# Performance work log

Hardware: AMD Instinct MI355X
Metric: run time of the kernel (lower is better)

## Reference

```python
import jax, jax.numpy as jnp
import numpy as np


def setup_inputs() -> dict:
    key = jax.random.key(0)
    ks = jax.random.split(key, 8)
    B, S, H, I = 2, 1025, 3200, 12800
    T = B * S
    # int8 tensors represented as int32, symmetric range [-128, 126]
    hidden_states = jax.random.randint(ks[0], (B, S, H), 0, 255, dtype=jnp.int32) - 127
    scale_in = (jax.random.uniform(ks[1], (T,)) * 0.02 + 1e-4).astype(jnp.float16)
    w1 = jax.random.randint(ks[2], (I, H), 0, 255, dtype=jnp.int32) - 127
    w1_scale = (jax.random.uniform(ks[3], (I,)) * 0.01 + 1e-4).astype(jnp.float32)
    b1 = (jax.random.normal(ks[4], (I,)) * 0.02).astype(jnp.float16)
    w2 = jax.random.randint(ks[5], (H, I), 0, 255, dtype=jnp.int32) - 127
    w2_scale = (jax.random.uniform(ks[6], (H,)) * 0.01 + 1e-4).astype(jnp.float32)
    b2 = (jax.random.normal(ks[7], (H,)) * 0.02).astype(jnp.float16)
    return {"hidden_states": hidden_states, "scale_in": scale_in,
            "w1": w1, "w1_scale": w1_scale, "b1": b1,
            "w2": w2, "w2_scale": w2_scale, "b2": b2}


def _w8a8_linear(x_int, scale_x, w_int, w_scale, bias):
    # int8 GEMM with int32 accumulation, dequant with per-token * per-channel scales
    acc = jnp.matmul(x_int, w_int.T)  # [T, out] int32
    out = acc.astype(jnp.float32) * scale_x[:, None].astype(jnp.float32) * w_scale[None, :]
    return (out + bias.astype(jnp.float32)).astype(jnp.float16)


def _gelu_and_quant(x_f16):
    # fused GELU + per-token dynamic symmetric int8 quantization
    g = jax.nn.gelu(x_f16.astype(jnp.float32), approximate=False)  # [T, I]
    amax = jnp.max(jnp.abs(g), axis=-1)                              # [T]
    scale_act = (amax / 127.0).astype(jnp.float16)
    s = jnp.maximum(scale_act.astype(jnp.float32), 1e-8)
    q = jnp.clip(jnp.round(g / s[:, None]), -128, 127).astype(jnp.int32)
    return q, scale_act


def reference(hidden_states, scale_in, w1, w1_scale, b1, w2, w2_scale, b2):
    B, S, H = hidden_states.shape
    x = hidden_states.reshape(-1, H)               # [T, H] int
    fc1_out = _w8a8_linear(x, scale_in, w1, w1_scale, b1)      # [T, I] fp16
    act_out, scale_act = _gelu_and_quant(fc1_out)              # int8-as-int32, [T] fp16
    fc2_out = _w8a8_linear(act_out, scale_act, w2, w2_scale, b2)  # [T, H] fp16
    return fc2_out
```

## Files before the change

### kernel.cpp

```cpp
#include <hip/hip_runtime.h>
#include <hip/hip_fp16.h>

typedef int v4i __attribute__((ext_vector_type(4)));

#define AS1C(p) ((const __attribute__((address_space(1))) void*)(p))
#define AS3(p)  ((__attribute__((address_space(3))) void*)(p))

__global__ void pack1(const int* __restrict__ a, const int* __restrict__ b,
                      signed char* __restrict__ pa, signed char* __restrict__ pb,
                      unsigned int* __restrict__ amax,
                      long long na, long long nb, int T) {
  const long long gid = blockIdx.x * (long long)blockDim.x + threadIdx.x;
  if (gid < T) amax[gid] = 0u;
  const long long n4a = na >> 2, n4b = nb >> 2;
  const long long tot = n4a + n4b;
  const long long stride = (long long)gridDim.x * blockDim.x;
  for (long long u = gid; u < tot; u += stride) {
    const int* src; signed char* dst; long long loc;
    if (u < n4a) { src = a; dst = pa; loc = u; }
    else         { src = b; dst = pb; loc = u - n4a; }
    const int4 v = *(const int4*)(src + (loc << 2));
    const unsigned out = (unsigned)(v.x & 0xff) | ((unsigned)(v.y & 0xff) << 8) |
                         ((unsigned)(v.z & 0xff) << 16) | ((unsigned)(v.w & 0xff) << 24);
    *(unsigned*)(dst + (loc << 2)) = out;
  }
}

__launch_bounds__(1024, 4)
__global__ void fc1_fused(const signed char* __restrict__ A, const signed char* __restrict__ Bw,
                          int M, int N, int K,
                          const float* __restrict__ scale_tok, const float* __restrict__ wsc,
                          const float* __restrict__ bias,
                          __half* __restrict__ gout, unsigned int* __restrict__ amax,
                          const int* __restrict__ w2src, signed char* __restrict__ w2dst,
                          long long n4w2, int npack, int gy) {
  __shared__ __align__(16) char smem[2][32768];
  const int bid = blockIdx.x;

  if (bid < npack) {
    const long long stride = (long long)npack * 1024;
    for (long long u = (long long)bid * 1024 + threadIdx.x; u < n4w2; u += stride) {
      const int4 v = *(const int4*)(w2src + (u << 2));
      const unsigned out = (unsigned)(v.x & 0xff) | ((unsigned)(v.y & 0xff) << 8) |
                           ((unsigned)(v.z & 0xff) << 16) | ((unsigned)(v.w & 0xff) << 24);
      *(unsigned*)(w2dst + (u << 2)) = out;
    }
    return;
  }

  const int tid = threadIdx.x;
  const int lane = tid & 63, wave = tid >> 6;
  const int wavem = wave >> 2, waven = wave & 3;
  const int lh = lane & 15, sseg = lane >> 4;

  int lid;
  {
    const int o = bid - npack;
    const int nwg = gridDim.x - npack;
    const int q = nwg >> 3, r = nwg & 7;
    const int x = o & 7, p = o >> 3;
    lid = (x < r ? x * (q + 1) : r * (q + 1) + (x - r) * q) + p;
  }
  const long long t0 = (long long)(lid % gy) * 256;
  const long long n0 = (long long)(lid / gy) * 256;
  const int nk = K >> 6;
  const long long Mm1 = M - 1, Nm1 = N - 1;

  const int lr4 = lane >> 2, slot = lane & 3;
  const int rloc = wave * 16 + lr4;
  const int gslot = (slot ^ ((rloc >> 1) & 3)) << 4;
  const signed char* sp0;
  const signed char* sp1;
  {
    long long gr = t0 + rloc; if (gr > Mm1) gr = Mm1;
    sp0 = A + gr * (long long)K + gslot;
    long long gn = n0 + rloc; if (gn > Nm1) gn = Nm1;
    sp1 = Bw + gn * (long long)K + gslot;
  }
  const int d0 = wave * 1024, d1 = 16384 + wave * 1024;

#define STAGE(bi) do { \
    __builtin_amdgcn_global_load_lds(AS1C(sp0), AS3(&smem[bi][d0]), 16, 0, 0); sp0 += 64; \
    __builtin_amdgcn_global_load_lds(AS1C(sp1), AS3(&smem[bi][d1]), 16, 0, 0); sp1 += 64; \
  } while (0)

  const int xs = ((sseg ^ ((lh >> 1) & 3)) << 4);
  const int offA = wavem * 4096 + lh * 64 + xs;
  const int offB = 16384 + waven * 4096 + lh * 64 + xs;

  v4i acc[4][4] = {};

  STAGE(0);
  __syncthreads();

  int cur = 0;
  for (int kt = 0; kt < nk; ++kt) {
    if (kt + 1 < nk) STAGE(cur ^ 1);
    const char* base = smem[cur];
    v4i af[4], bf[2];
#pragma unroll
    for (int mi = 0; mi < 4; ++mi) af[mi] = *(const v4i*)(base + offA + mi * 1024);
    bf[0] = *(const v4i*)(base + offB);
    bf[1] = *(const v4i*)(base + offB + 1024);
#pragma unroll
    for (int mi = 0; mi < 4; ++mi) {
      acc[mi][0] = __builtin_amdgcn_mfma_i32_16x16x64_i8(af[mi], bf[0], acc[mi][0], 0, 0, 0);
      acc[mi][1] = __builtin_amdgcn_mfma_i32_16x16x64_i8(af[mi], bf[1], acc[mi][1], 0, 0, 0);
    }
    bf[0] = *(const v4i*)(base + offB + 2048);
    bf[1] = *(const v4i*)(base + offB + 3072);
#pragma unroll
    for (int mi = 0; mi < 4; ++mi) {
      acc[mi][2] = __builtin_amdgcn_mfma_i32_16x16x64_i8(af[mi], bf[0], acc[mi][2], 0, 0, 0);
      acc[mi][3] = __builtin_amdgcn_mfma_i32_16x16x64_i8(af[mi], bf[1], acc[mi][3], 0, 0, 0);
    }
    __syncthreads();
    cur ^= 1;
  }
#undef STAGE

  long long cidx[4]; float w4[4], bi4[4]; bool cok[4];
#pragma unroll
  for (int ni = 0; ni < 4; ++ni) {
    cidx[ni] = n0 + waven * 64 + ni * 16 + lh;
    cok[ni] = cidx[ni] < N;
    w4[ni] = cok[ni] ? wsc[cidx[ni]] : 0.f;
    bi4[ni] = cok[ni] ? bias[cidx[ni]] : 0.f;
  }
#pragma unroll
  for (int mi = 0; mi < 4; ++mi) {
#pragma unroll
    for (int j = 0; j < 4; ++j) {
      const long long t = t0 + wavem * 64 + mi * 16 + (lane >> 4) * 4 + j;
      const bool valid = t < M;
      const float st = valid ? scale_tok[t] : 0.f;
      float rowmax = 0.f;
#pragma unroll
      for (int ni = 0; ni < 4; ++ni) {
        float v = (float)acc[mi][ni][j] * st * w4[ni] + bi4[ni];
        v = __half2float(__float2half(v));
        const float gl = 0.5f * v * (1.f + erff(v * 0.70710678118654752f));
        rowmax = fmaxf(rowmax, fabsf(gl));
        if (valid && cok[ni]) gout[t * (long long)N + cidx[ni]] = __float2half(gl);
      }
#pragma unroll
      for (int m = 1; m < 16; m <<= 1) rowmax = fmaxf(rowmax, __shfl_xor(rowmax, m));
      if (valid && lh == 0) atomicMax(&amax[t], __float_as_uint(rowmax));
    }
  }
}

__launch_bounds__(256, 4)
__global__ void gemm_fc2s(const signed char* __restrict__ A, const signed char* __restrict__ Bw,
                          int M, int N, int K, int* __restrict__ pbuf) {
  __shared__ __align__(16) char lds[2][2][128 * 64];
  const int tid = threadIdx.x;
  const int lane = tid & 63, wave = tid >> 6;
  const int wrow = (wave >> 1) * 64, wcol = (wave & 1) * 64;

  const int z = blockIdx.x & 1;
  const int o = blockIdx.x >> 1;
  const int gy = (M + 127) >> 7;
  const int nwg = gridDim.x >> 1;
  int lid;
  {
    const int q = nwg >> 3, r = nwg & 7;
    const int x = o & 7, p = o >> 3;
    lid = (x < r ? x * (q + 1) : r * (q + 1) + (x - r) * q) + p;
  }
  const long long t0 = (long long)(lid % gy) * 128;
  const long long n0 = (long long)(lid / gy) * 128;
  const int koff = z * (K >> 1);
  const int nk = (K >> 1) >> 6;
  const long long Mm1 = M - 1, Nm1 = N - 1;

  const signed char* sp[4];
  int dst[4];
#pragma unroll
  for (int i = 0; i < 4; ++i) {
    const bool isA = i < 2;
    const int c = wave * 2 + (i & 1);
    const int lr = c * 16 + (lane >> 2);
    const int gslot = (((lane & 3) ^ ((lr >> 1) & 3)) << 4);
    long long gr = (isA ? t0 : n0) + lr;
    const long long rmax = isA ? Mm1 : Nm1;
    if (gr > rmax) gr = rmax;
    sp[i] = (isA ? A : Bw) + gr * (long long)K + koff + gslot;
    dst[i] = (isA ? 0 : 8192) + c * 1024;
  }

#define STAGE(bi) do { \
    _Pragma("unroll") \
    for (int i = 0; i < 4; ++i) { \
      __builtin_amdgcn_global_load_lds(AS1C(sp[i]), AS3(&lds[bi][0][0] + dst[i]), 16, 0, 0); \
      sp[i] += 64; \
    } \
  } while (0)

  const int srow = lane & 15, sseg = lane >> 4;
  const int xs = ((sseg ^ ((srow >> 1) & 3)) << 4);
  const int offA = (wrow + srow) * 64 + xs;
  const int offB = 8192 + (wcol + srow) * 64 + xs;

  v4i acc[4][4] = {};

  STAGE(0);
  __syncthreads();

  int cur = 0;
  for (int kt = 0; kt < nk; ++kt) {
    if (kt + 1 < nk) STAGE(cur ^ 1);
    const char* base = &lds[cur][0][0];
    v4i af[4], bf[4];
#pragma unroll
    for (int mi = 0; mi < 4; ++mi) af[mi] = *(const v4i*)(base + offA + mi * 1024);
#pragma unroll
    for (int ni = 0; ni < 4; ++ni) bf[ni] = *(const v4i*)(base + offB + ni * 1024);
#pragma unroll
    for (int mi = 0; mi < 4; ++mi)
#pragma unroll
      for (int ni = 0; ni < 4; ++ni)
        acc[mi][ni] = __builtin_amdgcn_mfma_i32_16x16x64_i8(af[mi], bf[ni], acc[mi][ni], 0, 0, 0);
    __syncthreads();
    cur ^= 1;
  }
#undef STAGE

  const long long zbase = (long long)z * M * N;
#pragma unroll
  for (int mi = 0; mi < 4; ++mi) {
#pragma unroll
    for (int j = 0; j < 4; ++j) {
      const long long t = t0 + wrow + mi * 16 + (lane >> 4) * 4 + j;
      if (t < M) {
#pragma unroll
        for (int ni = 0; ni < 4; ++ni) {
          const long long c = n0 + wcol + ni * 16 + (lane & 15);
          pbuf[zbase + t * (long long)N + c] = acc[mi][ni][j];
        }
      }
    }
  }
}

__global__ void fc2_reduce(const int* __restrict__ pbuf, const unsigned int* __restrict__ amax,
                           const float* __restrict__ wsc, const float* __restrict__ bias,
                           float* __restrict__ out, int T_, int N_) {
  const long long MN = (long long)T_ * N_;
  const long long nchunk = MN >> 2;
  const long long stride = (long long)gridDim.x * blockDim.x;
  for (long long cchunk = blockIdx.x * (long long)blockDim.x + threadIdx.x;
       cchunk < nchunk; cchunk += stride) {
    const long long base = cchunk << 2;
    const int t = (int)(base / N_);
    const int n = (int)(base - (long long)t * N_);
    const float am = __uint_as_float(amax[t]);
    const float st = __half2float(__float2half(am * (1.f / 127.f)));
    const int4 p0 = *(const int4*)(pbuf + base);
    const int4 p1 = *(const int4*)(pbuf + MN + base);
    const float4 w = *(const float4*)(wsc + n);
    const float4 b = *(const float4*)(bias + n);
    float4 o;
    o.x = __half2float(__float2half((float)(p0.x + p1.x) * st * w.x + b.x));
    o.y = __half2float(__float2half((float)(p0.y + p1.y) * st * w.y + b.y));
    o.z = __half2float(__float2half((float)(p0.z + p1.z) * st * w.z + b.z));
    o.w = __half2float(__float2half((float)(p0.w + p1.w) * st * w.w + b.w));
    *(float4*)(out + base) = o;
  }
}

__global__ void gelu_quant(const __half* __restrict__ g, const unsigned int* __restrict__ amax,
                           signed char* __restrict__ q, long long total, int I) {
  const long long nchunk = total >> 3;
  const long long stride = (long long)gridDim.x * blockDim.x;
  for (long long c = blockIdx.x * (long long)blockDim.x + threadIdx.x; c < nchunk; c += stride) {
    const long long base = c << 3;
    const int t = (int)(base / I);
    const float am = __uint_as_float(amax[t]);
    const float s = fmaxf(__half2float(__float2half(am * (1.f / 127.f))), 1e-8f);
    const float inv = 1.f / s;
    const int4 raw = *(const int4*)(g + base);
    const __half2* h2 = (const __half2*)&raw;
    union { signed char b[8]; int2 v; } u;
#pragma unroll
    for (int k = 0; k < 4; ++k) {
      const float2 f = __half22float2(h2[k]);
      const float q0 = fminf(fmaxf(rintf(f.x * inv), -128.f), 127.f);
      const float q1 = fminf(fmaxf(rintf(f.y * inv), -128.f), 127.f);
      u.b[k * 2]     = (signed char)(int)q0;
      u.b[k * 2 + 1] = (signed char)(int)q1;
    }
    *(int2*)(q + base) = u.v;
  }
}

extern "C" void kernel_launch(void* const* d_in, const int* in_sizes, int n_in,
                              void* d_out, int out_size, void* d_ws, size_t ws_size,
                              hipStream_t stream) {
  const int* hs = (const int*)d_in[0];
  const float* scale_in = (const float*)d_in[1];
  const int* w1 = (const int*)d_in[2];
  const float* w1s = (const float*)d_in[3];
  const float* b1 = (const float*)d_in[4];
  const int* w2 = (const int*)d_in[5];
  const float* w2s = (const float*)d_in[6];
  const float* b2 = (const float*)d_in[7];

  const int T = in_sizes[1];
  const int I = in_sizes[3];
  const int H = in_sizes[6];

  char* ws = (char*)d_ws;
  unsigned int* amax = (unsigned int*)ws;
  signed char* px  = (signed char*)(ws + 16384);
  signed char* pw1 = px + (size_t)T * H;
  signed char* pw2 = pw1 + (size_t)I * H;
  __half* gbuf = (__half*)(pw2 + (size_t)H * I);
  signed char* qbuf = (signed char*)(gbuf + (size_t)T * I);
  int* pbuf = (int*)gbuf;

  const long long nx = (long long)T * H, nw1 = (long long)I * H, nw2 = (long long)H * I;

  pack1<<<2048, 256, 0, stream>>>(hs, w1, px, pw1, amax, nx, nw1, T);

  const int NPACK = 62;
  const int gy1 = (T + 255) / 256;
  const int gemmBlocks = (I / 256) * gy1;
  fc1_fused<<<NPACK + gemmBlocks, 1024, 0, stream>>>(
      px, pw1, T, I, H, scale_in, w1s, b1, gbuf, amax,
      w2, pw2, nw2 >> 2, NPACK, gy1);

  gelu_quant<<<2048, 256, 0, stream>>>(gbuf, amax, qbuf, (long long)T * I, I);

  const int tiles2 = (H / 128) * ((T + 127) / 128);
  gemm_fc2s<<<tiles2 * 2, 256, 0, stream>>>(qbuf, pw2, T, H, I, pbuf);

  fc2_reduce<<<2048, 256, 0, stream>>>(pbuf, amax, w2s, b2, (float*)d_out, T, H);
}
```

Measured before the change: 340.2 us.

## Fuse split-K reduction into fc2 GEMM via last-arriver atomic counter

Removes the separate fc2_reduce kernel. Each split-K tile pair now increments a per-tile counter, and the second block to finish reads its partner's partial sums from the buffer, adds its own register accumulators, applies the dequant scales and bias, and writes the final output. This saves a kernel launch and one full read and write pass over one partial buffer. In exchange it adds threadfence and atomic synchronisation, and the counters are zeroed by widening the init in pack1 to cover the control area.

```diff
diff --git a/kernel.cpp b/kernel.cpp
--- a/kernel.cpp
+++ b/kernel.cpp
@@ -8,10 +8,10 @@
 
 __global__ void pack1(const int* __restrict__ a, const int* __restrict__ b,
                       signed char* __restrict__ pa, signed char* __restrict__ pb,
-                      unsigned int* __restrict__ amax,
-                      long long na, long long nb, int T) {
+                      unsigned int* __restrict__ ctrl,
+                      long long na, long long nb) {
   const long long gid = blockIdx.x * (long long)blockDim.x + threadIdx.x;
-  if (gid < T) amax[gid] = 0u;
+  if (gid < 4096) ctrl[gid] = 0u;
   const long long n4a = na >> 2, n4b = nb >> 2;
   const long long tot = n4a + n4b;
   const long long stride = (long long)gridDim.x * blockDim.x;
@@ -152,8 +152,12 @@
 
 __launch_bounds__(256, 4)
 __global__ void gemm_fc2s(const signed char* __restrict__ A, const signed char* __restrict__ Bw,
-                          int M, int N, int K, int* __restrict__ pbuf) {
+                          int M, int N, int K, int* __restrict__ pbuf,
+                          const unsigned int* __restrict__ amax,
+                          const float* __restrict__ wsc, const float* __restrict__ bias,
+                          float* __restrict__ fout, unsigned int* __restrict__ cnt) {
   __shared__ __align__(16) char lds[2][2][128 * 64];
+  __shared__ unsigned int done_s;
   const int tid = threadIdx.x;
   const int lane = tid & 63, wave = tid >> 6;
   const int wrow = (wave >> 1) * 64, wcol = (wave & 1) * 64;
@@ -226,7 +230,8 @@
   }
 #undef STAGE
 
-  const long long zbase = (long long)z * M * N;
+  const long long MN = (long long)M * N;
+  const long long zbase = (long long)z * MN;
 #pragma unroll
   for (int mi = 0; mi < 4; ++mi) {
 #pragma unroll
@@ -241,31 +246,40 @@
       }
     }
   }
-}
-
-__global__ void fc2_reduce(const int* __restrict__ pbuf, const unsigned int* __restrict__ amax,
-                           const float* __restrict__ wsc, const float* __restrict__ bias,
-                           float* __restrict__ out, int T_, int N_) {
-  const long long MN = (long long)T_ * N_;
-  const long long nchunk = MN >> 2;
-  const long long stride = (long long)gridDim.x * blockDim.x;
-  for (long long cchunk = blockIdx.x * (long long)blockDim.x + threadIdx.x;
-       cchunk < nchunk; cchunk += stride) {
-    const long long base = cchunk << 2;
-    const int t = (int)(base / N_);
-    const int n = (int)(base - (long long)t * N_);
-    const float am = __uint_as_float(amax[t]);
-    const float st = __half2float(__float2half(am * (1.f / 127.f)));
-    const int4 p0 = *(const int4*)(pbuf + base);
-    const int4 p1 = *(const int4*)(pbuf + MN + base);
-    const float4 w = *(const float4*)(wsc + n);
-    const float4 b = *(const float4*)(bias + n);
-    float4 o;
-    o.x = __half2float(__float2half((float)(p0.x + p1.x) * st * w.x + b.x));
-    o.y = __half2float(__float2half((float)(p0.y + p1.y) * st * w.y + b.y));
-    o.z = __half2float(__float2half((float)(p0.z + p1.z) * st * w.z + b.z));
-    o.w = __half2float(__float2half((float)(p0.w + p1.w) * st * w.w + b.w));
-    *(float4*)(out + base) = o;
+
+  __threadfence();
+  __syncthreads();
+  if (tid == 0) done_s = atomicAdd(&cnt[o], 1u);
+  __syncthreads();
+
+  if (done_s == 1u) {
+    __threadfence();
+    const long long obase = (long long)(z ^ 1) * MN;
+    float w4[4], bi4[4];
+    long long cc[4];
+#pragma unroll
+    for (int ni = 0; ni < 4; ++ni) {
+      cc[ni] = n0 + wcol + ni * 16 + (lane & 15);
+      w4[ni] = wsc[cc[ni]];
+      bi4[ni] = bias[cc[ni]];
+    }
+#pragma unroll
+    for (int mi = 0; mi < 4; ++mi) {
+#pragma unroll
+      for (int j = 0; j < 4; ++j) {
+        const long long t = t0 + wrow + mi * 16 + (lane >> 4) * 4 + j;
+        if (t < M) {
+          const float am = __uint_as_float(amax[t]);
+          const float st = __half2float(__float2half(am * (1.f / 127.f)));
+#pragma unroll
+          for (int ni = 0; ni < 4; ++ni) {
+            const int other = pbuf[obase + t * (long long)N + cc[ni]];
+            const float v = (float)(acc[mi][ni][j] + other) * st * w4[ni] + bi4[ni];
+            fout[t * (long long)N + cc[ni]] = __half2float(__float2half(v));
+          }
+        }
+      }
+    }
   }
 }
 
@@ -312,6 +326,7 @@
 
   char* ws = (char*)d_ws;
   unsigned int* amax = (unsigned int*)ws;
+  unsigned int* cnt  = (unsigned int*)(ws + 12288);
   signed char* px  = (signed char*)(ws + 16384);
   signed char* pw1 = px + (size_t)T * H;
   signed char* pw2 = pw1 + (size_t)I * H;
@@ -321,7 +336,7 @@
 
   const long long nx = (long long)T * H, nw1 = (long long)I * H, nw2 = (long long)H * I;
 
-  pack1<<<2048, 256, 0, stream>>>(hs, w1, px, pw1, amax, nx, nw1, T);
+  pack1<<<2048, 256, 0, stream>>>(hs, w1, px, pw1, amax, nx, nw1);
 
   const int NPACK = 62;
   const int gy1 = (T + 255) / 256;
@@ -333,7 +348,6 @@
   gelu_quant<<<2048, 256, 0, stream>>>(gbuf, amax, qbuf, (long long)T * I, I);
 
   const int tiles2 = (H / 128) * ((T + 127) / 128);
-  gemm_fc2s<<<tiles2 * 2, 256, 0, stream>>>(qbuf, pw2, T, H, I, pbuf);
-
-  fc2_reduce<<<2048, 256, 0, stream>>>(pbuf, amax, w2s, b2, (float*)d_out, T, H);
-}
+  gemm_fc2s<<<tiles2 * 2, 256, 0, stream>>>(qbuf, pw2, T, H, I, pbuf,
+                                            amax, w2s, b2, (float*)d_out, cnt);
+}
```

Result: slower. 570.3 us (+67.7%).
